# Kernel optimization log

Hardware: AMD Instinct MI355X
Metric: run time of the kernel (lower is better)

## Reference

```python
import jax, jax.numpy as jnp
import numpy as np

N, C, TX, TY = 32, 256, 1024, 1024


def setup_inputs() -> dict:
    key = jax.random.key(0)
    ks = jax.random.split(key, 9)
    s = 1.0 / np.sqrt(C)
    return {
        "Q": jax.random.normal(ks[0], (N, C, TY), dtype=jnp.float32),
        "K": jax.random.normal(ks[1], (N, C, TX), dtype=jnp.float32),
        "V": jax.random.normal(ks[2], (N, C, TX), dtype=jnp.float32),
        "Wq": jax.random.normal(ks[3], (C, C), dtype=jnp.float32) * s,
        "bq": jax.random.normal(ks[4], (C,), dtype=jnp.float32) * 0.01,
        "Wk": jax.random.normal(ks[5], (C, C), dtype=jnp.float32) * s,
        "bk": jax.random.normal(ks[6], (C,), dtype=jnp.float32) * 0.01,
        "Wv": jax.random.normal(ks[7], (C, C), dtype=jnp.float32) * s,
        "bv": jax.random.normal(ks[8], (C,), dtype=jnp.float32) * 0.01,
    }


def _proj_tanh(W, b, x):
    # 1x1 conv over channels: (C_out, C_in) x (N, C_in, T) -> (N, C_out, T)
    return jnp.tanh(jnp.einsum("oc,nct->not", W, x) + b[None, :, None])


def reference(Q, K, V, Wq, bq, Wk, bk, Wv, bv):
    d_k = Q.shape[1]
    Qp = _proj_tanh(Wq, bq, Q)  # (N, C, Ty)
    Kp = _proj_tanh(Wk, bk, K)  # (N, C, Tx)
    Vp = _proj_tanh(Wv, bv, V)  # (N, C, Tx)
    scores = jnp.einsum("ncs,nct->nst", Kp, Qp) / jnp.sqrt(
        jnp.asarray(d_k, dtype=Q.dtype)
    )  # (N, Tx, Ty)
    A = jax.nn.softmax(scores, axis=1)  # softmax over Tx (dim=1)
    R = jnp.einsum("ncs,nst->nct", Vp, A)  # (N, C, Ty)
    return (R, A)
```

## Files before the change

kernel.cpp:

```cpp
#include <hip/hip_runtime.h>
#include <stdint.h>

#define N_B 32
#define C_D 256
#define T_D 1024

typedef unsigned short u16;
typedef __attribute__((ext_vector_type(8))) short short8;
typedef __attribute__((ext_vector_type(4))) float f32x4;

__device__ __forceinline__ u16 f2bf(float f) {
    unsigned x = __float_as_uint(f);
    return (u16)((x + 0x7fffu + ((x >> 16) & 1u)) >> 16);
}

__device__ __forceinline__ void gld16(const void* g, void* l) {
    __builtin_amdgcn_global_load_lds(
        (const __attribute__((address_space(1))) uint32_t*)g,
        (__attribute__((address_space(3))) uint32_t*)l, 16, 0, 0);
}

__device__ __forceinline__ void comb(float& m, float& l, float m2, float l2) {
    float M = fmaxf(m, m2);
    l = l * __expf(m - M) + l2 * __expf(m2 - M);
    m = M;
}

__global__ __launch_bounds__(256) void conv_w(const float* __restrict__ w0,
                                              const float* __restrict__ w1,
                                              const float* __restrict__ w2,
                                              u16* __restrict__ o0,
                                              u16* __restrict__ o1,
                                              u16* __restrict__ o2) {
    const float* in = blockIdx.y == 0 ? w0 : (blockIdx.y == 1 ? w1 : w2);
    u16* out       = blockIdx.y == 0 ? o0 : (blockIdx.y == 1 ? o1 : o2);
    int i = blockIdx.x * 256 + threadIdx.x;
    out[i] = f2bf(in[i]);
}

template <bool NORM>
__device__ __forceinline__ void stage_tr(const float* __restrict__ src,
                                         u16* __restrict__ sm, int tid,
                                         const float* Mv, const float* Rv,
                                         float* adst, bool awr) {
    const int sr2 = tid >> 4;
    const int tt8 = (tid & 15) * 8;
    float4 v0 = *(const float4*)(src);
    float4 v1 = *(const float4*)(src + 4);
    float4 w0 = *(const float4*)(src + T_D);
    float4 w1 = *(const float4*)(src + T_D + 4);
    float a[8] = {v0.x, v0.y, v0.z, v0.w, v1.x, v1.y, v1.z, v1.w};
    float b[8] = {w0.x, w0.y, w0.z, w0.w, w1.x, w1.y, w1.z, w1.w};
    if constexpr (NORM) {
#pragma unroll
        for (int j = 0; j < 8; ++j) {
            a[j] = __expf(a[j] - Mv[j]) * Rv[j];
            b[j] = __expf(b[j] - Mv[j]) * Rv[j];
        }
        if (awr) {
            ((float4*)adst)[0]         = make_float4(a[0], a[1], a[2], a[3]);
            ((float4*)adst)[1]         = make_float4(a[4], a[5], a[6], a[7]);
            ((float4*)(adst + T_D))[0] = make_float4(b[0], b[1], b[2], b[3]);
            ((float4*)(adst + T_D))[1] = make_float4(b[4], b[5], b[6], b[7]);
        }
    }
    const int kk = sr2 * 2;
#pragma unroll
    for (int j = 0; j < 8; ++j) {
        const int t  = tt8 + j;
        const int ks = kk ^ (((t >> 4) & 3) << 3);
        uint32_t pk = (uint32_t)f2bf(a[j]) | ((uint32_t)f2bf(b[j]) << 16);
        *(uint32_t*)(sm + t * 32 + ks) = pk;
    }
}

template <bool TRA, bool TRB, int EPI, bool F32OUT, bool NORM>
__global__ __launch_bounds__(256) void gemm_t(
        const void* __restrict__ Av, const void* __restrict__ Bv,
        const float* __restrict__ bias, void* __restrict__ OutV,
        int Kdim, int ldo, long sA, long sB, long sO, float scale,
        float* __restrict__ Pm, float* __restrict__ Pl,
        const float* __restrict__ Mf, const float* __restrict__ Rl,
        float* __restrict__ Aw)
{
    __shared__ __align__(16) u16 smA[128 * 32];
    __shared__ __align__(16) u16 smB[128 * 32];

    const int nb = blockIdx.z;
    const int n0 = blockIdx.x * 128;
    const int m0 = blockIdx.y * 128;
    const int tid = threadIdx.x;

    const int srow = tid >> 2;
    const int sk8  = (tid & 3) * 8;
    const int sr2  = tid >> 4;
    const int tt8  = (tid & 15) * 8;

    const u16* gA0 = nullptr; const u16* gA1 = nullptr;
    const float* tA = nullptr;
    if constexpr (TRA) {
        tA = (const float*)Av + (size_t)nb * sA + (size_t)(sr2 * 2) * T_D + m0 + tt8;
    } else {
        const u16* Ab = (const u16*)Av + (size_t)nb * sA;
        gA0 = Ab + (size_t)(m0 + srow) * Kdim + sk8;
        gA1 = gA0 + (size_t)64 * Kdim;
    }
    const u16* gB0 = nullptr; const u16* gB1 = nullptr;
    const float* tB = nullptr;
    if constexpr (TRB) {
        tB = (const float*)Bv + (size_t)nb * sB + (size_t)(sr2 * 2) * T_D + n0 + tt8;
    } else {
        const u16* Bb = (const u16*)Bv + (size_t)nb * sB;
        gB0 = Bb + (size_t)(n0 + srow) * Kdim + sk8;
        gB1 = gB0 + (size_t)64 * Kdim;
    }
    u16* lA0 = smA + tid * 8; u16* lA1 = smA + 2048 + tid * 8;
    u16* lB0 = smB + tid * 8; u16* lB1 = smB + 2048 + tid * 8;

    float Mv[8], Rv[8];
    float* awbase = nullptr;
    bool awr = false;
    if constexpr (NORM) {
#pragma unroll
        for (int j = 0; j < 8; ++j) {
            Mv[j] = Mf[(size_t)nb * T_D + n0 + tt8 + j];
            Rv[j] = Rl[(size_t)nb * T_D + n0 + tt8 + j];
        }
        awbase = Aw + (size_t)nb * sB + (size_t)(sr2 * 2) * T_D + n0 + tt8;
        awr = (blockIdx.y == 0);
    }

    const int lane = tid & 63;
    const int w    = tid >> 6;
    const int wm   = (w >> 1) * 64;
    const int wn   = (w & 1) * 64;
    const int l15  = lane & 15;
    const int quad = lane >> 4;

    f32x4 acc[4][4];
#pragma unroll
    for (int i = 0; i < 4; ++i)
#pragma unroll
        for (int j = 0; j < 4; ++j) acc[i][j] = (f32x4){0.f, 0.f, 0.f, 0.f};

    for (int kb = 0; kb < Kdim; kb += 32) {
        if constexpr (TRA) {
            stage_tr<false>(tA + (size_t)kb * T_D, smA, tid, nullptr, nullptr, nullptr, false);
        } else {
            gld16(gA0 + kb, lA0);
            gld16(gA1 + kb, lA1);
        }
        if constexpr (TRB) {
            if constexpr (NORM)
                stage_tr<true>(tB + (size_t)kb * T_D, smB, tid, Mv, Rv,
                               awbase + (size_t)kb * T_D, awr);
            else
                stage_tr<false>(tB + (size_t)kb * T_D, smB, tid, nullptr, nullptr, nullptr, false);
        } else {
            gld16(gB0 + kb, lB0);
            gld16(gB1 + kb, lB1);
        }
        __syncthreads();
        short8 af[4], bfr[4];
#pragma unroll
        for (int i = 0; i < 4; ++i) {
            const int ra = wm + i * 16 + l15;
            const int ca = TRA ? ((quad ^ ((ra >> 4) & 3)) * 8) : (quad * 8);
            af[i] = *(const short8*)(smA + ra * 32 + ca);
            const int rb = wn + i * 16 + l15;
            const int cb = TRB ? ((quad ^ ((rb >> 4) & 3)) * 8) : (quad * 8);
            bfr[i] = *(const short8*)(smB + rb * 32 + cb);
        }
#pragma unroll
        for (int mi = 0; mi < 4; ++mi)
#pragma unroll
            for (int ni = 0; ni < 4; ++ni)
                acc[mi][ni] = __builtin_amdgcn_mfma_f32_16x16x32_bf16(
                        af[mi], bfr[ni], acc[mi][ni], 0, 0, 0);
        __syncthreads();
    }

    if constexpr (EPI == 3) {
        float pmv[4] = {-1e30f, -1e30f, -1e30f, -1e30f};
        float plv[4] = {0.f, 0.f, 0.f, 0.f};
#pragma unroll
        for (int mi = 0; mi < 4; ++mi) {
            const int mb = m0 + wm + mi * 16 + quad * 4;
#pragma unroll
            for (int r = 0; r < 4; ++r) {
                const int m = mb + r;
#pragma unroll
                for (int ni = 0; ni < 4; ++ni) {
                    const int nn = n0 + wn + ni * 16 + l15;
                    float v = acc[mi][ni][r] * scale;
                    ((float*)OutV)[(size_t)nb * sO + (size_t)m * ldo + nn] = v;
                    pmv[ni] = fmaxf(pmv[ni], v);
                }
            }
        }
#pragma unroll
        for (int ni = 0; ni < 4; ++ni) {
            float s = 0.f;
#pragma unroll
            for (int mi = 0; mi < 4; ++mi)
#pragma unroll
                for (int r = 0; r < 4; ++r)
                    s += __expf(acc[mi][ni][r] * scale - pmv[ni]);
            plv[ni] = s;
        }
#pragma unroll
        for (int ni = 0; ni < 4; ++ni) {
            float m = pmv[ni], l = plv[ni];
            float m2 = __shfl_xor(m, 16), l2 = __shfl_xor(l, 16);
            comb(m, l, m2, l2);
            m2 = __shfl_xor(m, 32); l2 = __shfl_xor(l, 32);
            comb(m, l, m2, l2);
            pmv[ni] = m; plv[ni] = l;
        }
        __shared__ float red_m[4][64];
        __shared__ float red_l[4][64];
        if (quad == 0) {
#pragma unroll
            for (int ni = 0; ni < 4; ++ni) {
                red_m[w][ni * 16 + l15] = pmv[ni];
                red_l[w][ni * 16 + l15] = plv[ni];
            }
        }
        __syncthreads();
        if (tid < 128) {
            const int half = tid >> 6, cc = tid & 63;
            float m = red_m[half][cc], l = red_l[half][cc];
            comb(m, l, red_m[half + 2][cc], red_l[half + 2][cc]);
            const size_t pi = ((size_t)nb * 8 + blockIdx.y) * T_D + n0 + tid;
            Pm[pi] = m; Pl[pi] = l;
        }
    } else {
#pragma unroll
        for (int mi = 0; mi < 4; ++mi) {
            const int mb = m0 + wm + mi * 16 + quad * 4;
#pragma unroll
            for (int r = 0; r < 4; ++r) {
                const int m = mb + r;
                float bm = 0.f;
                if (EPI == 2) bm = bias[m];
#pragma unroll
                for (int ni = 0; ni < 4; ++ni) {
                    const int nn = n0 + wn + ni * 16 + l15;
                    float v = acc[mi][ni][r] * scale;
                    if (EPI == 1) v = tanhf(v + bias[nn]);
                    if (EPI == 2) v = tanhf(v + bm);
                    if (F32OUT)
                        ((float*)OutV)[(size_t)nb * sO + (size_t)m * ldo + nn] = v;
                    else
                        ((u16*)OutV)[(size_t)nb * sO + (size_t)m * ldo + nn] = f2bf(v);
                }
            }
        }
    }
}

__global__ __launch_bounds__(256) void merge_ml(const float* __restrict__ Pm,
                                                const float* __restrict__ Pl,
                                                float* __restrict__ Mf,
                                                float* __restrict__ Rl) {
    const int i = blockIdx.x * 256 + threadIdx.x;
    const int n = i >> 10, t = i & (T_D - 1);
    const float* pm = Pm + (size_t)n * 8 * T_D + t;
    const float* pl = Pl + (size_t)n * 8 * T_D + t;
    float M = -1e30f;
#pragma unroll
    for (int j = 0; j < 8; ++j) M = fmaxf(M, pm[(size_t)j * T_D]);
    float L = 0.f;
#pragma unroll
    for (int j = 0; j < 8; ++j) L += pl[(size_t)j * T_D] * __expf(pm[(size_t)j * T_D] - M);
    Mf[i] = M;
    Rl[i] = 1.0f / L;
}

__global__ __launch_bounds__(256) void norm_a(float* __restrict__ S,
                                              const float* __restrict__ Mf,
                                              const float* __restrict__ Rl) {
    const size_t i = ((size_t)blockIdx.x * 256 + threadIdx.x) * 4;
    const int n = (int)(i >> 20);
    const int t = (int)(i & (T_D - 1));
    float4 M = *(const float4*)(Mf + (size_t)n * T_D + t);
    float4 R = *(const float4*)(Rl + (size_t)n * T_D + t);
    float4 v = *(float4*)(S + i);
    v.x = __expf(v.x - M.x) * R.x;
    v.y = __expf(v.y - M.y) * R.y;
    v.z = __expf(v.z - M.z) * R.z;
    v.w = __expf(v.w - M.w) * R.w;
    *(float4*)(S + i) = v;
}

__global__ __launch_bounds__(256) void softmax_cols(float* __restrict__ S) {
    __shared__ float pm[16][64];
    __shared__ float pl[16][64];
    __shared__ float fM[64];
    __shared__ float fR[64];
    const int n   = blockIdx.y;
    const int t0  = blockIdx.x * 64;
    const int tid = threadIdx.x;
    const int g   = tid >> 4;
    const int ci  = (tid & 15) * 4;
    float* A = S + (size_t)n * T_D * T_D + t0 + ci;
    float* p = A + (size_t)g * 64 * T_D;

    float m[4] = {-1e30f, -1e30f, -1e30f, -1e30f};
    float l[4] = {0.f, 0.f, 0.f, 0.f};
#pragma unroll 8
    for (int s = 0; s < 64; ++s) {
        float4 v = *(const float4*)(p + (size_t)s * T_D);
        float x[4] = {v.x, v.y, v.z, v.w};
#pragma unroll
        for (int j = 0; j < 4; ++j) {
            float nm = fmaxf(m[j], x[j]);
            l[j] = l[j] * __expf(m[j] - nm) + __expf(x[j] - nm);
            m[j] = nm;
        }
    }
#pragma unroll
    for (int j = 0; j < 4; ++j) { pm[g][ci + j] = m[j]; pl[g][ci + j] = l[j]; }
    __syncthreads();
    if (tid < 64) {
        float M = -1e30f;
#pragma unroll
        for (int g2 = 0; g2 < 16; ++g2) M = fmaxf(M, pm[g2][tid]);
        float L = 0.f;
#pragma unroll
        for (int g2 = 0; g2 < 16; ++g2) L += pl[g2][tid] * __expf(pm[g2][tid] - M);
        fM[tid] = M;
        fR[tid] = 1.0f / L;
    }
    __syncthreads();
    float M[4], R[4];
#pragma unroll
    for (int j = 0; j < 4; ++j) { M[j] = fM[ci + j]; R[j] = fR[ci + j]; }
#pragma unroll 8
    for (int s = 0; s < 64; ++s) {
        float4 v = *(const float4*)(p + (size_t)s * T_D);
        v.x = __expf(v.x - M[0]) * R[0];
        v.y = __expf(v.y - M[1]) * R[1];
        v.z = __expf(v.z - M[2]) * R[2];
        v.w = __expf(v.w - M[3]) * R[3];
        *(float4*)(p + (size_t)s * T_D) = v;
    }
}

extern "C" void kernel_launch(void* const* d_in, const int* in_sizes, int n_in,
                              void* d_out, int out_size, void* d_ws, size_t ws_size,
                              hipStream_t stream) {
    const float* Qf = (const float*)d_in[0];
    const float* Kf = (const float*)d_in[1];
    const float* Vf = (const float*)d_in[2];
    const float* Wq = (const float*)d_in[3];
    const float* bq = (const float*)d_in[4];
    const float* Wk = (const float*)d_in[5];
    const float* bk = (const float*)d_in[6];
    const float* Wv = (const float*)d_in[7];
    const float* bv = (const float*)d_in[8];

    float* Rout = (float*)d_out;
    float* Aout = Rout + (size_t)N_B * C_D * T_D;

    u16* QpT = (u16*)Rout;
    u16* KpT = (u16*)Rout + 8388608;
    u16* Wqb = (u16*)Aout;
    u16* Wkb = Wqb + 65536;
    u16* Wvb = Wkb + 65536;
    u16* Vp  = (u16*)d_in[0];

    dim3 blk(256);
    const long sX = (long)C_D * T_D;
    const long sS = (long)T_D * T_D;

    const size_t elemsS = (size_t)N_B * T_D * T_D;
    const size_t elemsP = (size_t)N_B * 8 * T_D;
    const size_t elemsM = (size_t)N_B * T_D;
    const size_t needA = (elemsS + 2 * elemsP + 2 * elemsM) * 4;
    const size_t needB = (2 * elemsP + 2 * elemsM) * 4;

    conv_w<<<dim3(256, 3), blk, 0, stream>>>(Wq, Wk, Wv, Wqb, Wkb, Wvb);

    gemm_t<true, false, 1, false, false><<<dim3(2, 8, N_B), blk, 0, stream>>>(
            Qf, Wqb, bq, QpT, C_D, C_D, sX, 0, sX, 1.0f,
            nullptr, nullptr, nullptr, nullptr, nullptr);
    gemm_t<true, false, 1, false, false><<<dim3(2, 8, N_B), blk, 0, stream>>>(
            Kf, Wkb, bk, KpT, C_D, C_D, sX, 0, sX, 1.0f,
            nullptr, nullptr, nullptr, nullptr, nullptr);
    gemm_t<false, true, 2, false, false><<<dim3(8, 2, N_B), blk, 0, stream>>>(
            Wvb, Vf, bv, Vp, C_D, T_D, 0, sX, sX, 1.0f,
            nullptr, nullptr, nullptr, nullptr, nullptr);

    if (ws_size >= needA) {
        float* Sws = (float*)d_ws;
        float* Pm  = Sws + elemsS;
        float* Pl  = Pm + elemsP;
        float* Mf  = Pl + elemsP;
        float* Rl  = Mf + elemsM;
        gemm_t<false, false, 3, true, false><<<dim3(8, 8, N_B), blk, 0, stream>>>(
                KpT, QpT, nullptr, Sws, C_D, T_D, sX, sX, sS, 0.0625f,
                Pm, Pl, nullptr, nullptr, nullptr);
        merge_ml<<<dim3(128), blk, 0, stream>>>(Pm, Pl, Mf, Rl);
        gemm_t<false, true, 0, true, true><<<dim3(8, 2, N_B), blk, 0, stream>>>(
                Vp, Sws, nullptr, Rout, T_D, T_D, sX, sS, sX, 1.0f,
                nullptr, nullptr, Mf, Rl, Aout);
    } else if (ws_size >= needB) {
        float* Pm = (float*)d_ws;
        float* Pl = Pm + elemsP;
        float* Mf = Pl + elemsP;
        float* Rl = Mf + elemsM;
        gemm_t<false, false, 3, true, false><<<dim3(8, 8, N_B), blk, 0, stream>>>(
                KpT, QpT, nullptr, Aout, C_D, T_D, sX, sX, sS, 0.0625f,
                Pm, Pl, nullptr, nullptr, nullptr);
        merge_ml<<<dim3(128), blk, 0, stream>>>(Pm, Pl, Mf, Rl);
        norm_a<<<dim3(32768), blk, 0, stream>>>(Aout, Mf, Rl);
        gemm_t<false, true, 0, true, false><<<dim3(8, 2, N_B), blk, 0, stream>>>(
                Vp, Aout, nullptr, Rout, T_D, T_D, sX, sS, sX, 1.0f,
                nullptr, nullptr, nullptr, nullptr, nullptr);
    } else {
        gemm_t<false, false, 0, true, false><<<dim3(8, 8, N_B), blk, 0, stream>>>(
                KpT, QpT, nullptr, Aout, C_D, T_D, sX, sX, sS, 0.0625f,
                nullptr, nullptr, nullptr, nullptr, nullptr);
        softmax_cols<<<dim3(16, N_B), blk, 0, stream>>>(Aout);
        gemm_t<false, true, 0, true, false><<<dim3(8, 2, N_B), blk, 0, stream>>>(
                Vp, Aout, nullptr, Rout, T_D, T_D, sX, sS, sX, 1.0f,
                nullptr, nullptr, nullptr, nullptr, nullptr);
    }
}
```

Measured before the change: 418.8 us.

## Fuse softmax normalization in place into full-channel R GEMM, drop workspace paths

```diff
diff --git a/kernel.cpp b/kernel.cpp
--- a/kernel.cpp
+++ b/kernel.cpp
@@ -39,8 +39,7 @@
 }
 
 template <bool NORM>
-__device__ __forceinline__ void stage_tr(const float* __restrict__ src,
-                                         u16* __restrict__ sm, int tid,
+__device__ __forceinline__ void stage_tr(const float* src, u16* sm, int tid,
                                          const float* Mv, const float* Rv,
                                          float* adst, bool awr) {
     const int sr2 = tid >> 4;
@@ -74,14 +73,12 @@
     }
 }
 
-template <bool TRA, bool TRB, int EPI, bool F32OUT, bool NORM>
+template <bool TRA, bool TRB, int EPI, bool F32OUT>
 __global__ __launch_bounds__(256) void gemm_t(
         const void* __restrict__ Av, const void* __restrict__ Bv,
         const float* __restrict__ bias, void* __restrict__ OutV,
         int Kdim, int ldo, long sA, long sB, long sO, float scale,
-        float* __restrict__ Pm, float* __restrict__ Pl,
-        const float* __restrict__ Mf, const float* __restrict__ Rl,
-        float* __restrict__ Aw)
+        float* __restrict__ Pm, float* __restrict__ Pl)
 {
     __shared__ __align__(16) u16 smA[128 * 32];
     __shared__ __align__(16) u16 smB[128 * 32];
@@ -117,19 +114,6 @@
     u16* lA0 = smA + tid * 8; u16* lA1 = smA + 2048 + tid * 8;
     u16* lB0 = smB + tid * 8; u16* lB1 = smB + 2048 + tid * 8;
 
-    float Mv[8], Rv[8];
-    float* awbase = nullptr;
-    bool awr = false;
-    if constexpr (NORM) {
-#pragma unroll
-        for (int j = 0; j < 8; ++j) {
-            Mv[j] = Mf[(size_t)nb * T_D + n0 + tt8 + j];
-            Rv[j] = Rl[(size_t)nb * T_D + n0 + tt8 + j];
-        }
-        awbase = Aw + (size_t)nb * sB + (size_t)(sr2 * 2) * T_D + n0 + tt8;
-        awr = (blockIdx.y == 0);
-    }
-
     const int lane = tid & 63;
     const int w    = tid >> 6;
     const int wm   = (w >> 1) * 64;
@@ -151,11 +135,7 @@
             gld16(gA1 + kb, lA1);
         }
         if constexpr (TRB) {
-            if constexpr (NORM)
-                stage_tr<true>(tB + (size_t)kb * T_D, smB, tid, Mv, Rv,
-                               awbase + (size_t)kb * T_D, awr);
-            else
-                stage_tr<false>(tB + (size_t)kb * T_D, smB, tid, nullptr, nullptr, nullptr, false);
+            stage_tr<false>(tB + (size_t)kb * T_D, smB, tid, nullptr, nullptr, nullptr, false);
         } else {
             gld16(gB0 + kb, lB0);
             gld16(gB1 + kb, lB1);
@@ -277,73 +257,91 @@
     Rl[i] = 1.0f / L;
 }
 
-__global__ __launch_bounds__(256) void norm_a(float* __restrict__ S,
-                                              const float* __restrict__ Mf,
-                                              const float* __restrict__ Rl) {
-    const size_t i = ((size_t)blockIdx.x * 256 + threadIdx.x) * 4;
-    const int n = (int)(i >> 20);
-    const int t = (int)(i & (T_D - 1));
-    float4 M = *(const float4*)(Mf + (size_t)n * T_D + t);
-    float4 R = *(const float4*)(Rl + (size_t)n * T_D + t);
-    float4 v = *(float4*)(S + i);
-    v.x = __expf(v.x - M.x) * R.x;
-    v.y = __expf(v.y - M.y) * R.y;
-    v.z = __expf(v.z - M.z) * R.z;
-    v.w = __expf(v.w - M.w) * R.w;
-    *(float4*)(S + i) = v;
-}
-
-__global__ __launch_bounds__(256) void softmax_cols(float* __restrict__ S) {
-    __shared__ float pm[16][64];
-    __shared__ float pl[16][64];
-    __shared__ float fM[64];
-    __shared__ float fR[64];
-    const int n   = blockIdx.y;
-    const int t0  = blockIdx.x * 64;
+__global__ __launch_bounds__(512) void gemm_rn(
+        const u16* __restrict__ Vp, float* S,
+        const float* __restrict__ Mf, const float* __restrict__ Rl,
+        float* __restrict__ R)
+{
+    __shared__ __align__(16) u16 smA[256 * 32];
+    __shared__ __align__(16) u16 smB[128 * 32];
+
+    const int nb  = blockIdx.z;
+    const int n0  = blockIdx.x * 128;
     const int tid = threadIdx.x;
-    const int g   = tid >> 4;
-    const int ci  = (tid & 15) * 4;
-    float* A = S + (size_t)n * T_D * T_D + t0 + ci;
-    float* p = A + (size_t)g * 64 * T_D;
-
-    float m[4] = {-1e30f, -1e30f, -1e30f, -1e30f};
-    float l[4] = {0.f, 0.f, 0.f, 0.f};
-#pragma unroll 8
-    for (int s = 0; s < 64; ++s) {
-        float4 v = *(const float4*)(p + (size_t)s * T_D);
-        float x[4] = {v.x, v.y, v.z, v.w};
-#pragma unroll
-        for (int j = 0; j < 4; ++j) {
-            float nm = fmaxf(m[j], x[j]);
-            l[j] = l[j] * __expf(m[j] - nm) + __expf(x[j] - nm);
-            m[j] = nm;
-        }
-    }
-#pragma unroll
-    for (int j = 0; j < 4; ++j) { pm[g][ci + j] = m[j]; pl[g][ci + j] = l[j]; }
-    __syncthreads();
-    if (tid < 64) {
-        float M = -1e30f;
-#pragma unroll
-        for (int g2 = 0; g2 < 16; ++g2) M = fmaxf(M, pm[g2][tid]);
-        float L = 0.f;
-#pragma unroll
-        for (int g2 = 0; g2 < 16; ++g2) L += pl[g2][tid] * __expf(pm[g2][tid] - M);
-        fM[tid] = M;
-        fR[tid] = 1.0f / L;
-    }
-    __syncthreads();
-    float M[4], R[4];
-#pragma unroll
-    for (int j = 0; j < 4; ++j) { M[j] = fM[ci + j]; R[j] = fR[ci + j]; }
-#pragma unroll 8
-    for (int s = 0; s < 64; ++s) {
-        float4 v = *(const float4*)(p + (size_t)s * T_D);
-        v.x = __expf(v.x - M[0]) * R[0];
-        v.y = __expf(v.y - M[1]) * R[1];
-        v.z = __expf(v.z - M[2]) * R[2];
-        v.w = __expf(v.w - M[3]) * R[3];
-        *(float4*)(p + (size_t)s * T_D) = v;
+
+    const u16* Ab = Vp + (size_t)nb * (C_D * T_D);
+    float* Sb = S + (size_t)nb * ((size_t)T_D * T_D);
+    float* Rb = R + (size_t)nb * (C_D * T_D);
+
+    const int srow = tid >> 2;
+    const int sk8  = (tid & 3) * 8;
+    const u16* gA0 = Ab + (size_t)srow * T_D + sk8;
+    const u16* gA1 = gA0 + (size_t)128 * T_D;
+    u16* lA0 = smA + tid * 8;
+    u16* lA1 = smA + 4096 + tid * 8;
+
+    float Mv[8], Rv[8];
+    float* tB = nullptr;
+    if (tid < 256) {
+        const int sr2 = tid >> 4;
+        const int tt8 = (tid & 15) * 8;
+        tB = Sb + (size_t)(sr2 * 2) * T_D + n0 + tt8;
+#pragma unroll
+        for (int j = 0; j < 8; ++j) {
+            Mv[j] = Mf[(size_t)nb * T_D + n0 + tt8 + j];
+            Rv[j] = Rl[(size_t)nb * T_D + n0 + tt8 + j];
+        }
+    }
+
+    const int lane = tid & 63;
+    const int w    = tid >> 6;
+    const int wm   = (w >> 1) * 64;
+    const int wn   = (w & 1) * 64;
+    const int l15  = lane & 15;
+    const int quad = lane >> 4;
+
+    f32x4 acc[4][4];
+#pragma unroll
+    for (int i = 0; i < 4; ++i)
+#pragma unroll
+        for (int j = 0; j < 4; ++j) acc[i][j] = (f32x4){0.f, 0.f, 0.f, 0.f};
+
+    for (int kb = 0; kb < T_D; kb += 32) {
+        gld16(gA0 + kb, lA0);
+        gld16(gA1 + kb, lA1);
+        if (tid < 256) {
+            float* src = tB + (size_t)kb * T_D;
+            stage_tr<true>(src, smB, tid, Mv, Rv, src, true);
+        }
+        __syncthreads();
+        short8 af[4], bfr[4];
+#pragma unroll
+        for (int i = 0; i < 4; ++i) {
+            af[i] = *(const short8*)(smA + (wm + i * 16 + l15) * 32 + quad * 8);
+            const int rb = wn + i * 16 + l15;
+            bfr[i] = *(const short8*)(smB + rb * 32 + ((quad ^ ((rb >> 4) & 3)) * 8));
+        }
+#pragma unroll
+        for (int mi = 0; mi < 4; ++mi)
+#pragma unroll
+            for (int ni = 0; ni < 4; ++ni)
+                acc[mi][ni] = __builtin_amdgcn_mfma_f32_16x16x32_bf16(
+                        af[mi], bfr[ni], acc[mi][ni], 0, 0, 0);
+        __syncthreads();
+    }
+
+#pragma unroll
+    for (int mi = 0; mi < 4; ++mi) {
+        const int mb = wm + mi * 16 + quad * 4;
+#pragma unroll
+        for (int r = 0; r < 4; ++r) {
+            const int m = mb + r;
+#pragma unroll
+            for (int ni = 0; ni < 4; ++ni) {
+                const int nn = n0 + wn + ni * 16 + l15;
+                Rb[(size_t)m * T_D + nn] = acc[mi][ni][r];
+            }
+        }
     }
 }
 
@@ -370,61 +368,28 @@
     u16* Wvb = Wkb + 65536;
     u16* Vp  = (u16*)d_in[0];
 
+    float* Pm = (float*)d_in[1];
+    float* Pl = Pm + (size_t)N_B * 8 * T_D;
+    float* Mf = Pl + (size_t)N_B * 8 * T_D;
+    float* Rl = Mf + (size_t)N_B * T_D;
+
     dim3 blk(256);
     const long sX = (long)C_D * T_D;
     const long sS = (long)T_D * T_D;
 
-    const size_t elemsS = (size_t)N_B * T_D * T_D;
-    const size_t elemsP = (size_t)N_B * 8 * T_D;
-    const size_t elemsM = (size_t)N_B * T_D;
-    const size_t needA = (elemsS + 2 * elemsP + 2 * elemsM) * 4;
-    const size_t needB = (2 * elemsP + 2 * elemsM) * 4;
-
     conv_w<<<dim3(256, 3), blk, 0, stream>>>(Wq, Wk, Wv, Wqb, Wkb, Wvb);
 
-    gemm_t<true, false, 1, false, false><<<dim3(2, 8, N_B), blk, 0, stream>>>(
-            Qf, Wqb, bq, QpT, C_D, C_D, sX, 0, sX, 1.0f,
-            nullptr, nullptr, nullptr, nullptr, nullptr);
-    gemm_t<true, false, 1, false, false><<<dim3(2, 8, N_B), blk, 0, stream>>>(
-            Kf, Wkb, bk, KpT, C_D, C_D, sX, 0, sX, 1.0f,
-            nullptr, nullptr, nullptr, nullptr, nullptr);
-    gemm_t<false, true, 2, false, false><<<dim3(8, 2, N_B), blk, 0, stream>>>(
-            Wvb, Vf, bv, Vp, C_D, T_D, 0, sX, sX, 1.0f,
-            nullptr, nullptr, nullptr, nullptr, nullptr);
-
-    if (ws_size >= needA) {
-        float* Sws = (float*)d_ws;
-        float* Pm  = Sws + elemsS;
-        float* Pl  = Pm + elemsP;
-        float* Mf  = Pl + elemsP;
-        float* Rl  = Mf + elemsM;
-        gemm_t<false, false, 3, true, false><<<dim3(8, 8, N_B), blk, 0, stream>>>(
-                KpT, QpT, nullptr, Sws, C_D, T_D, sX, sX, sS, 0.0625f,
-                Pm, Pl, nullptr, nullptr, nullptr);
-        merge_ml<<<dim3(128), blk, 0, stream>>>(Pm, Pl, Mf, Rl);
-        gemm_t<false, true, 0, true, true><<<dim3(8, 2, N_B), blk, 0, stream>>>(
-                Vp, Sws, nullptr, Rout, T_D, T_D, sX, sS, sX, 1.0f,
-                nullptr, nullptr, Mf, Rl, Aout);
-    } else if (ws_size >= needB) {
-        float* Pm = (float*)d_ws;
-        float* Pl = Pm + elemsP;
-        float* Mf = Pl + elemsP;
-        float* Rl = Mf + elemsM;
-        gemm_t<false, false, 3, true, false><<<dim3(8, 8, N_B), blk, 0, stream>>>(
-                KpT, QpT, nullptr, Aout, C_D, T_D, sX, sX, sS, 0.0625f,
-                Pm, Pl, nullptr, nullptr, nullptr);
-        merge_ml<<<dim3(128), blk, 0, stream>>>(Pm, Pl, Mf, Rl);
-        norm_a<<<dim3(32768), blk, 0, stream>>>(Aout, Mf, Rl);
-        gemm_t<false, true, 0, true, false><<<dim3(8, 2, N_B), blk, 0, stream>>>(
-                Vp, Aout, nullptr, Rout, T_D, T_D, sX, sS, sX, 1.0f,
-                nullptr, nullptr, nullptr, nullptr, nullptr);
-    } else {
-        gemm_t<false, false, 0, true, false><<<dim3(8, 8, N_B), blk, 0, stream>>>(
-                KpT, QpT, nullptr, Aout, C_D, T_D, sX, sX, sS, 0.0625f,
-                nullptr, nullptr, nullptr, nullptr, nullptr);
-        softmax_cols<<<dim3(16, N_B), blk, 0, stream>>>(Aout);
-        gemm_t<false, true, 0, true, false><<<dim3(8, 2, N_B), blk, 0, stream>>>(
-                Vp, Aout, nullptr, Rout, T_D, T_D, sX, sS, sX, 1.0f,
-                nullptr, nullptr, nullptr, nullptr, nullptr);
-    }
-}
+    gemm_t<true, false, 1, false><<<dim3(2, 8, N_B), blk, 0, stream>>>(
+            Qf, Wqb, bq, QpT, C_D, C_D, sX, 0, sX, 1.0f, nullptr, nullptr);
+    gemm_t<true, false, 1, false><<<dim3(2, 8, N_B), blk, 0, stream>>>(
+            Kf, Wkb, bk, KpT, C_D, C_D, sX, 0, sX, 1.0f, nullptr, nullptr);
+    gemm_t<false, true, 2, false><<<dim3(8, 2, N_B), blk, 0, stream>>>(
+            Wvb, Vf, bv, Vp, C_D, T_D, 0, sX, sX, 1.0f, nullptr, nullptr);
+
+    gemm_t<false, false, 3, true><<<dim3(8, 8, N_B), blk, 0, stream>>>(
+            KpT, QpT, nullptr, Aout, C_D, T_D, sX, sX, sS, 0.0625f, Pm, Pl);
+
+    merge_ml<<<dim3(128), blk, 0, stream>>>(Pm, Pl, Mf, Rl);
+
+    gemm_rn<<<dim3(8, 1, N_B), dim3(512), 0, stream>>>(Vp, Aout, Mf, Rl, Rout);
+}
```

Measured after the change: 389.7 us. -6.9%, faster.
